# Kernel optimization log

Measured on AMD Instinct MI355X. Metric: run time of the kernel, lower is better.

## Reference

```python
import jax, jax.numpy as jnp
import numpy as np
import math

D_MODEL, D_ENC, D_K, D_V, N_HEADS = 1024, 1024, 64, 64, 16
B, LQ, LK = 8, 1024, 1024


def setup_inputs() -> dict:
    key = jax.random.key(0)
    ks = jax.random.split(key, 9)
    # per-head Q/K/V linear params, stacked over heads (torch Linear: y = x @ W^T + b;
    # we store W already transposed as [in, out])
    lim_q = 1.0 / math.sqrt(D_MODEL)
    lim_e = 1.0 / math.sqrt(D_ENC)
    return {
        "decoder_batch": jax.random.normal(ks[0], (B, LQ, D_MODEL), jnp.float32),
        "encoder_out": jax.random.normal(ks[1], (B, LK, D_ENC), jnp.float32),
        "attn_mask": jax.random.randint(ks[2], (B, LQ, LK), 0, 2, jnp.int32),
        "Wq": jax.random.uniform(ks[3], (N_HEADS, D_MODEL, D_K), jnp.float32, -lim_q, lim_q),
        "bq": jax.random.uniform(ks[4], (N_HEADS, D_K), jnp.float32, -lim_q, lim_q),
        "Wk": jax.random.uniform(ks[5], (N_HEADS, D_ENC, D_K), jnp.float32, -lim_e, lim_e),
        "bk": jax.random.uniform(ks[6], (N_HEADS, D_K), jnp.float32, -lim_e, lim_e),
        "Wv": jax.random.uniform(ks[7], (N_HEADS, D_ENC, D_V), jnp.float32, -lim_e, lim_e),
        "bv": jax.random.uniform(ks[8], (N_HEADS, D_V), jnp.float32, -lim_e, lim_e),
    }


def reference(decoder_batch, encoder_out, attn_mask, Wq, bq, Wk, bk, Wv, bv):
    # Batched-over-heads version of the per-head Python loop (same math).
    q = jnp.einsum("bqd,hdk->bhqk", decoder_batch, Wq) + bq[None, :, None, :]
    k = jnp.einsum("bsd,hdk->bhsk", encoder_out, Wk) + bk[None, :, None, :]
    v = jnp.einsum("bsd,hdv->bhsv", encoder_out, Wv) + bv[None, :, None, :]
    scale = 1.0 / math.sqrt(D_K)
    logits = jnp.einsum("bhqk,bhsk->bhqs", q, k) * scale  # [B,H,LQ,LK]
    masked = attn_mask[:, None, :, :] == 0  # broadcast over heads
    # -inf mask; -1e30 yields exactly-zero probs for masked entries in fp32
    logits = jnp.where(masked, jnp.float32(-1e30), logits)
    scores = jax.nn.softmax(logits, axis=-1)
    # NaN fix: rows with all positions masked become all-zero (matches scores[scores!=scores]=0)
    all_masked = jnp.all(masked, axis=-1, keepdims=True)
    scores = jnp.where(all_masked, jnp.float32(0.0), scores)
    # dropout_prob=0.0 (eval) -> identity
    out = jnp.einsum("bhqs,bhsv->bhqv", scores, v)  # [B,H,LQ,D_V]
    # concat heads on last dim: [B,LQ,H*D_V]
    return out.transpose(0, 2, 1, 3).reshape(B, LQ, N_HEADS * D_V)
```

## Files before the change

### kernel.cpp

```cpp
#include <hip/hip_runtime.h>
#include <hip/hip_bf16.h>
#include <stdint.h>

#define DM   1024
#define DKV  64
#define NH   16
#define NB   8
#define SLEN 1024

typedef float  f32x4  __attribute__((ext_vector_type(4)));
typedef __bf16 bf16x8 __attribute__((ext_vector_type(8)));

#define L2E 1.44269504089f

__device__ __forceinline__ void gload_lds16(const void* g, void* l) {
  __builtin_amdgcn_global_load_lds(
      (const __attribute__((address_space(1))) void*)g,
      (__attribute__((address_space(3))) void*)l, 16, 0, 0);
}

__device__ __forceinline__ unsigned short f2bf(float f) {
  uint32_t u = __builtin_bit_cast(uint32_t, f);
  u += 0x7fffu + ((u >> 16) & 1u);
  return (unsigned short)(u >> 16);
}

__global__ void k_wT(const float* __restrict__ Wq, const float* __restrict__ Wk,
                     const float* __restrict__ Wv, unsigned short* __restrict__ Tq,
                     unsigned short* __restrict__ Tk, unsigned short* __restrict__ Tv) {
  __shared__ float tile[64][65];
  const int t = threadIdx.x;
  const int dc = blockIdx.x, h = blockIdx.y, s = blockIdx.z;
  const float* W = (s == 0) ? Wq : (s == 1) ? Wk : Wv;
  unsigned short* T = (s == 0) ? Tq : (s == 1) ? Tk : Tv;
#pragma unroll
  for (int i = 0; i < 4; ++i) {
    int idx = i * 256 + t;
    int d = idx >> 4, kg = idx & 15;
    float4 v = *(const float4*)(W + ((size_t)h * DM + dc * 64 + d) * DKV + kg * 4);
    tile[d][kg * 4 + 0] = v.x; tile[d][kg * 4 + 1] = v.y;
    tile[d][kg * 4 + 2] = v.z; tile[d][kg * 4 + 3] = v.w;
  }
  __syncthreads();
  int k = t >> 2, dg = t & 3;
  union { unsigned short u[8]; int4 v; } o0, o1;
#pragma unroll
  for (int j = 0; j < 8; ++j) o0.u[j] = f2bf(tile[dg * 16 + j][k]);
#pragma unroll
  for (int j = 0; j < 8; ++j) o1.u[j] = f2bf(tile[dg * 16 + 8 + j][k]);
  unsigned short* dst = T + ((size_t)h * DKV + k) * DM + dc * 64 + dg * 16;
  *(int4*)dst = o0.v;
  *(int4*)(dst + 8) = o1.v;
}

__global__ void k_pack(const int* __restrict__ m, uint32_t* __restrict__ out) {
  int wi = blockIdx.x * 256 + threadIdx.x;
  const int* p = m + (size_t)wi * 32;
  uint32_t bits = 0;
#pragma unroll
  for (int i = 0; i < 8; ++i) {
    int4 v = *(const int4*)(p + i * 4);
    bits |= ((uint32_t)(v.x != 0)) << (i * 4 + 0);
    bits |= ((uint32_t)(v.y != 0)) << (i * 4 + 1);
    bits |= ((uint32_t)(v.z != 0)) << (i * 4 + 2);
    bits |= ((uint32_t)(v.w != 0)) << (i * 4 + 3);
  }
  out[wi] = bits;
}

template <int EPI>
__global__ __launch_bounds__(256, 2)
void k_gemmF(const float* __restrict__ A, const unsigned short* __restrict__ BT,
             const float* __restrict__ bias, unsigned short* __restrict__ C) {
  __shared__ char As[8192];
  __shared__ char Bs[8192];
  const int t = threadIdx.x;
  const int w = t >> 6, lane = t & 63;
  const int g = lane >> 4, r16 = lane & 15;
  const int wm = w >> 1, wn = w & 1;
  const int m0 = blockIdx.y * 128, n0 = blockIdx.x * 128;
  const int arow = t >> 2, ac = t & 3;

  f32x4 acc[4][4] = {};
  for (int kt = 0; kt < DM / 32; ++kt) {
    float4 a0[2], a1[2];
#pragma unroll
    for (int i = 0; i < 2; ++i) {
      const float* src = A + (size_t)(m0 + arow + i * 64) * DM + kt * 32 + ac * 8;
      a0[i] = *(const float4*)src;
      a1[i] = *(const float4*)(src + 4);
    }
    __syncthreads();
#pragma unroll
    for (int i = 0; i < 2; ++i) {
      int row = arow + i * 64;
      int pos = ac ^ (row & 3);
      gload_lds16(BT + (size_t)(n0 + row) * DM + kt * 32 + pos * 8,
                  Bs + i * 4096 + w * 1024);
      union { unsigned short u[8]; int4 v; } o;
      o.u[0] = f2bf(a0[i].x); o.u[1] = f2bf(a0[i].y);
      o.u[2] = f2bf(a0[i].z); o.u[3] = f2bf(a0[i].w);
      o.u[4] = f2bf(a1[i].x); o.u[5] = f2bf(a1[i].y);
      o.u[6] = f2bf(a1[i].z); o.u[7] = f2bf(a1[i].w);
      *(int4*)(As + row * 64 + (pos << 4)) = o.v;
    }
    __syncthreads();
    bf16x8 af[4], bfr[4];
#pragma unroll
    for (int m = 0; m < 4; ++m) {
      int row = wm * 64 + m * 16 + r16;
      af[m] = *(const bf16x8*)(As + row * 64 + ((g ^ (row & 3)) << 4));
    }
#pragma unroll
    for (int n = 0; n < 4; ++n) {
      int row = wn * 64 + n * 16 + r16;
      bfr[n] = *(const bf16x8*)(Bs + row * 64 + ((g ^ (row & 3)) << 4));
    }
#pragma unroll
    for (int m = 0; m < 4; ++m)
#pragma unroll
      for (int n = 0; n < 4; ++n)
        acc[m][n] = __builtin_amdgcn_mfma_f32_16x16x32_bf16(af[m], bfr[n], acc[m][n], 0, 0, 0);
  }
#pragma unroll
  for (int m = 0; m < 4; ++m) {
    int rowb = m0 + wm * 64 + m * 16 + 4 * g;
#pragma unroll
    for (int n = 0; n < 4; ++n) {
      int col = n0 + wn * 64 + n * 16 + r16;
      float bv = bias[col];
      if (EPI == 0) {
#pragma unroll
        for (int r = 0; r < 4; ++r)
          C[(size_t)(rowb + r) * DM + col] = f2bf(acc[m][n][r] + bv);
      } else {
        int b = rowb >> 10, s = rowb & 1023;
        int h = col >> 6, v = col & 63;
        union { unsigned short u[4]; ushort4 q; } o;
#pragma unroll
        for (int r = 0; r < 4; ++r) o.u[r] = f2bf(acc[m][n][r] + bv);
        *(ushort4*)(C + (((size_t)(b * NH + h) * DKV + v) << 10) + s) = o.q;
      }
    }
  }
}

__global__ __launch_bounds__(256, 2)
void k_attn(const unsigned short* __restrict__ Q, const unsigned short* __restrict__ K,
            const unsigned short* __restrict__ VT, const uint32_t* __restrict__ MP,
            float* __restrict__ O) {
  __shared__ char Ks[8192];
  __shared__ char Vs[8192];
  __shared__ char Ps[8192];
  const int t = threadIdx.x, w = t >> 6, lane = t & 63;
  const int g = lane >> 4, r16 = lane & 15;
  const int qt = blockIdx.x, bh = blockIdx.y;
  const int b = bh >> 4, h = bh & 15;
  const int q0 = qt * 64 + w * 16;
  const int q = q0 + r16;
  const int g4 = g * 4;
  const int x7 = r16 & 7;

  bf16x8 aq[2];
#pragma unroll
  for (int kc = 0; kc < 2; ++kc)
    aq[kc] = *(const bf16x8*)(Q + (size_t)(b * SLEN + q) * DM + h * DKV + kc * 32 + g * 8);

  f32x4 oacc[4] = {};
  float mrun = -1e30f, lrun = 0.f;
  const float SCL = 0.125f * L2E;

  const unsigned short* Kbase = K  + (size_t)b * SLEN * DM + h * DKV;
  const unsigned short* Vbase = VT + (size_t)bh * DKV * SLEN;
  const uint32_t*       Mlane = MP + (size_t)(b * SLEN + q) * 32;
  char* PsW = Ps + w * 2048 + r16 * 128;

  for (int st = 0; st < 16; ++st) {
    const int s0 = st * 64;
    uint32_t mw0 = Mlane[(s0 >> 5) + 0] >> g4;
    uint32_t mw1 = Mlane[(s0 >> 5) + 1] >> g4;
    __syncthreads();
#pragma unroll
    for (int i = 0; i < 2; ++i) {
      int row  = (t >> 3) + i * 32;
      int slot = (t & 7) ^ (row & 7);
      gload_lds16(Kbase + (size_t)(s0 + row) * DM + slot * 8, Ks + i * 4096 + w * 1024);
      gload_lds16(Vbase + (size_t)row * SLEN + s0 + slot * 8, Vs + i * 4096 + w * 1024);
    }
    __syncthreads();

    f32x4 sacc[4];
#pragma unroll
    for (int f = 0; f < 4; ++f) {
      sacc[f] = (f32x4){0.f, 0.f, 0.f, 0.f};
#pragma unroll
      for (int kc = 0; kc < 2; ++kc) {
        bf16x8 bk_ = *(const bf16x8*)(Ks + (f * 16 + r16) * 128 + (((kc * 4 + g) ^ x7) << 4));
        sacc[f] = __builtin_amdgcn_mfma_f32_16x16x32_bf16(bk_, aq[kc], sacc[f], 0, 0, 0);
      }
    }

#pragma unroll
    for (int f = 0; f < 4; ++f) {
      uint32_t mwf = (f < 2) ? mw0 : mw1;
#pragma unroll
      for (int r = 0; r < 4; ++r) {
        uint32_t bit = (mwf >> (((f & 1) << 4) + r)) & 1u;
        sacc[f][r] = bit ? sacc[f][r] * SCL : -1e30f;
      }
    }
    float tm0 = fmaxf(fmaxf(sacc[0][0], sacc[0][1]), fmaxf(sacc[0][2], sacc[0][3]));
    float tm1 = fmaxf(fmaxf(sacc[1][0], sacc[1][1]), fmaxf(sacc[1][2], sacc[1][3]));
    float tm2 = fmaxf(fmaxf(sacc[2][0], sacc[2][1]), fmaxf(sacc[2][2], sacc[2][3]));
    float tm3 = fmaxf(fmaxf(sacc[3][0], sacc[3][1]), fmaxf(sacc[3][2], sacc[3][3]));
    float mt = fmaxf(fmaxf(tm0, tm1), fmaxf(tm2, tm3));
    mt = fmaxf(mt, __shfl_xor(mt, 16));
    mt = fmaxf(mt, __shfl_xor(mt, 32));

    float mnew = fmaxf(mrun, mt);
    float corr = __builtin_amdgcn_exp2f(mrun - mnew);
#pragma unroll
    for (int f = 0; f < 4; ++f)
#pragma unroll
      for (int r = 0; r < 4; ++r)
        sacc[f][r] = __builtin_amdgcn_exp2f(sacc[f][r] - mnew);
    float ts0 = (sacc[0][0] + sacc[0][1]) + (sacc[0][2] + sacc[0][3]);
    float ts1 = (sacc[1][0] + sacc[1][1]) + (sacc[1][2] + sacc[1][3]);
    float ts2 = (sacc[2][0] + sacc[2][1]) + (sacc[2][2] + sacc[2][3]);
    float ts3 = (sacc[3][0] + sacc[3][1]) + (sacc[3][2] + sacc[3][3]);
    float lt = (ts0 + ts1) + (ts2 + ts3);
    lt += __shfl_xor(lt, 16);
    lt += __shfl_xor(lt, 32);
    lrun = lrun * corr + lt;
    mrun = mnew;
#pragma unroll
    for (int n = 0; n < 4; ++n) oacc[n] *= corr;

#pragma unroll
    for (int f = 0; f < 4; ++f) {
      uint32_t lo, hi;
      asm("v_cvt_pk_bf16_f32 %0, %1, %2" : "=v"(lo) : "v"(sacc[f][0]), "v"(sacc[f][1]));
      asm("v_cvt_pk_bf16_f32 %0, %1, %2" : "=v"(hi) : "v"(sacc[f][2]), "v"(sacc[f][3]));
      int slot = ((f << 2) | g) ^ (x7 << 1);
      uint2 pk; pk.x = lo; pk.y = hi;
      *(uint2*)(PsW + slot * 8) = pk;
    }
    bf16x8 pa[2];
#pragma unroll
    for (int kc = 0; kc < 2; ++kc)
      pa[kc] = *(const bf16x8*)(PsW + (((kc * 4 + g) ^ x7) << 4));

#pragma unroll
    for (int n = 0; n < 4; ++n)
#pragma unroll
      for (int kc = 0; kc < 2; ++kc) {
        bf16x8 bv_ = *(const bf16x8*)(Vs + (n * 16 + r16) * 128 + (((kc * 4 + g) ^ x7) << 4));
        oacc[n] = __builtin_amdgcn_mfma_f32_16x16x32_bf16(bv_, pa[kc], oacc[n], 0, 0, 0);
      }
  }

  float inv = (mrun > -5e29f) ? (1.f / lrun) : 0.f;
  float* Orow = O + (size_t)(b * SLEN + q) * (NH * DKV) + h * DKV;
#pragma unroll
  for (int n = 0; n < 4; ++n) {
    float4 o4;
    o4.x = oacc[n][0] * inv; o4.y = oacc[n][1] * inv;
    o4.z = oacc[n][2] * inv; o4.w = oacc[n][3] * inv;
    *(float4*)(Orow + n * 16 + g4) = o4;
  }
}

extern "C" void kernel_launch(void* const* d_in, const int* in_sizes, int n_in,
                              void* d_out, int out_size, void* d_ws, size_t ws_size,
                              hipStream_t stream) {
  const float* dec = (const float*)d_in[0];
  const float* enc = (const float*)d_in[1];
  const int*   msk = (const int*)d_in[2];
  const float* Wq  = (const float*)d_in[3];
  const float* bq  = (const float*)d_in[4];
  const float* Wk  = (const float*)d_in[5];
  const float* bk  = (const float*)d_in[6];
  const float* Wv  = (const float*)d_in[7];
  const float* bv  = (const float*)d_in[8];
  float* out = (float*)d_out;

  char* ws = (char*)d_ws;
  const size_t MB = 1ull << 20;
  unsigned short* Tq = (unsigned short*)(ws + 0);
  unsigned short* Tk = (unsigned short*)(ws + 2 * MB);
  unsigned short* Tv = (unsigned short*)(ws + 4 * MB);
  uint32_t*       MP = (uint32_t*)(ws + 6 * MB);
  unsigned short* Qb = (unsigned short*)(ws + 7 * MB);
  unsigned short* Kb = (unsigned short*)(ws + 23 * MB);
  unsigned short* VT = (unsigned short*)(ws + 39 * MB);

  k_wT<<<dim3(16, 16, 3), dim3(256), 0, stream>>>(Wq, Wk, Wv, Tq, Tk, Tv);
  k_pack<<<dim3(1024), dim3(256), 0, stream>>>(msk, MP);
  k_gemmF<0><<<dim3(8, 64), dim3(256), 0, stream>>>(dec, Tq, bq, Qb);
  k_gemmF<0><<<dim3(8, 64), dim3(256), 0, stream>>>(enc, Tk, bk, Kb);
  k_gemmF<1><<<dim3(8, 64), dim3(256), 0, stream>>>(enc, Tv, bv, VT);
  k_attn<<<dim3(16, 128), dim3(256), 0, stream>>>(Qb, Kb, VT, MP, out);
}
```

Baseline: 344.5 us.

## Double-buffer LDS in projection GEMM and use packed bf16 conversion

Restructures the fp32-input projection GEMM main loop to double-buffer the A and B tiles in LDS. The next tile is staged and the tile after that is prefetched into registers while the current one is consumed, which drops one barrier per iteration. The change also replaces the software round-to-nearest fp32-to-bf16 conversion with the hardware v_cvt_pk_bf16_f32 instruction. LDS use per block doubles to 32KB, which could limit occupancy, and the prefetched registers raise register pressure.

```diff
diff --git a/kernel.cpp b/kernel.cpp
--- a/kernel.cpp
+++ b/kernel.cpp
@@ -72,8 +72,8 @@
 __global__ __launch_bounds__(256, 2)
 void k_gemmF(const float* __restrict__ A, const unsigned short* __restrict__ BT,
              const float* __restrict__ bias, unsigned short* __restrict__ C) {
-  __shared__ char As[8192];
-  __shared__ char Bs[8192];
+  __shared__ char As[16384];
+  __shared__ char Bs[16384];
   const int t = threadIdx.x;
   const int w = t >> 6, lane = t & 63;
   const int g = lane >> 4, r16 = lane & 15;
@@ -81,40 +81,55 @@
   const int m0 = blockIdx.y * 128, n0 = blockIdx.x * 128;
   const int arow = t >> 2, ac = t & 3;
 
-  f32x4 acc[4][4] = {};
-  for (int kt = 0; kt < DM / 32; ++kt) {
-    float4 a0[2], a1[2];
+  float4 a0[2], a1[2];
+
+  auto LOADA = [&](int kt) {
 #pragma unroll
     for (int i = 0; i < 2; ++i) {
       const float* src = A + (size_t)(m0 + arow + i * 64) * DM + kt * 32 + ac * 8;
       a0[i] = *(const float4*)src;
       a1[i] = *(const float4*)(src + 4);
     }
-    __syncthreads();
+  };
+  auto STAGE = [&](int kt) {
+    const int buf = (kt & 1) << 13;
 #pragma unroll
     for (int i = 0; i < 2; ++i) {
       int row = arow + i * 64;
       int pos = ac ^ (row & 3);
       gload_lds16(BT + (size_t)(n0 + row) * DM + kt * 32 + pos * 8,
-                  Bs + i * 4096 + w * 1024);
-      union { unsigned short u[8]; int4 v; } o;
-      o.u[0] = f2bf(a0[i].x); o.u[1] = f2bf(a0[i].y);
-      o.u[2] = f2bf(a0[i].z); o.u[3] = f2bf(a0[i].w);
-      o.u[4] = f2bf(a1[i].x); o.u[5] = f2bf(a1[i].y);
-      o.u[6] = f2bf(a1[i].z); o.u[7] = f2bf(a1[i].w);
-      *(int4*)(As + row * 64 + (pos << 4)) = o.v;
-    }
+                  Bs + buf + i * 4096 + w * 1024);
+      union { uint32_t u[4]; int4 v; } o;
+      asm("v_cvt_pk_bf16_f32 %0, %1, %2" : "=v"(o.u[0]) : "v"(a0[i].x), "v"(a0[i].y));
+      asm("v_cvt_pk_bf16_f32 %0, %1, %2" : "=v"(o.u[1]) : "v"(a0[i].z), "v"(a0[i].w));
+      asm("v_cvt_pk_bf16_f32 %0, %1, %2" : "=v"(o.u[2]) : "v"(a1[i].x), "v"(a1[i].y));
+      asm("v_cvt_pk_bf16_f32 %0, %1, %2" : "=v"(o.u[3]) : "v"(a1[i].z), "v"(a1[i].w));
+      *(int4*)(As + buf + row * 64 + (pos << 4)) = o.v;
+    }
+  };
+
+  f32x4 acc[4][4] = {};
+  const int NKT = DM / 32;
+  LOADA(0);
+  STAGE(0);
+  LOADA(1);
+  for (int kt = 0; kt < NKT; ++kt) {
     __syncthreads();
+    if (kt + 1 < NKT) {
+      STAGE(kt + 1);
+      if (kt + 2 < NKT) LOADA(kt + 2);
+    }
+    const int buf = (kt & 1) << 13;
     bf16x8 af[4], bfr[4];
 #pragma unroll
     for (int m = 0; m < 4; ++m) {
       int row = wm * 64 + m * 16 + r16;
-      af[m] = *(const bf16x8*)(As + row * 64 + ((g ^ (row & 3)) << 4));
+      af[m] = *(const bf16x8*)(As + buf + row * 64 + ((g ^ (row & 3)) << 4));
     }
 #pragma unroll
     for (int n = 0; n < 4; ++n) {
       int row = wn * 64 + n * 16 + r16;
-      bfr[n] = *(const bf16x8*)(Bs + row * 64 + ((g ^ (row & 3)) << 4));
+      bfr[n] = *(const bf16x8*)(Bs + buf + row * 64 + ((g ^ (row & 3)) << 4));
     }
 #pragma unroll
     for (int m = 0; m < 4; ++m)
```

Result: no change. 345.3 us (+0.2%).
